# Optimization experiments

Measured on AMD Instinct MI355X. Metric: run time of the kernel, lower is better.

Reference implementation:

```python
import jax, jax.numpy as jnp
import numpy as np

jax.config.update("jax_enable_x64", True)  # hash math uses int64, matching torch promotion

NUM_LEVELS = 16
MIN_RES = 16
MAX_RES = 1024
LOG2_T = 19
T = 2 ** LOG2_T          # hash table size per level
FEATS = 2                # features per level
HASH_INIT_SCALE = 0.001
N = 524288               # number of query points

# 8 cube corners; bit==1 selects ceil coordinate (weight = offset), bit==0 selects floor (weight = 1-offset)
CORNER_BITS = np.array([[(b >> 2) & 1, (b >> 1) & 1, b & 1] for b in range(8)], dtype=np.int64)
PRIMES = np.array([1, 2654435761, 805459861], dtype=np.int64)


def setup_inputs() -> dict:
    key = jax.random.key(0)
    k1, k2 = jax.random.split(key)
    x = jax.random.uniform(k1, (N, 3), dtype=jnp.float32, minval=-1.0, maxval=1.0)
    hash_table = (jax.random.uniform(k2, (T * NUM_LEVELS, FEATS), dtype=jnp.float32) * 2.0 - 1.0) * HASH_INIT_SCALE
    return {"x": x, "hash_table": hash_table}


def reference(x, hash_table):
    # per-level resolutions: floor(min_res * growth^level)
    growth = np.exp((np.log(MAX_RES) - np.log(MIN_RES)) / (NUM_LEVELS - 1))
    scalings = jnp.asarray(np.floor(MIN_RES * growth ** np.arange(NUM_LEVELS)), dtype=jnp.float32)  # [L]
    hash_offset = jnp.arange(NUM_LEVELS, dtype=jnp.int64) * T  # [L]

    x01 = x * 0.5 + 0.5                                # map [-1,1] -> [0,1]
    scaled = x01[..., None, :] * scalings[:, None]     # [N, L, 3]
    sc = jnp.ceil(scaled).astype(jnp.int64)            # [N, L, 3]
    sf = jnp.floor(scaled).astype(jnp.int64)           # [N, L, 3]
    offset = scaled - sf.astype(scaled.dtype)          # [N, L, 3] in [0,1)

    bits = jnp.asarray(CORNER_BITS)                    # [8, 3]
    # corner integer coords: [N, L, 8, 3]
    corners = jnp.where(bits[None, None] == 1, sc[:, :, None, :], sf[:, :, None, :])

    # Instant-NGP spatial hash (int64, matching torch's type promotion)
    p = corners * jnp.asarray(PRIMES)
    h = jnp.bitwise_xor(jnp.bitwise_xor(p[..., 0], p[..., 1]), p[..., 2])
    h = h % T + hash_offset[None, :, None]             # [N, L, 8]

    # trilinear weights: prod over dims of (offset if ceil else 1-offset)
    w = jnp.prod(jnp.where(bits[None, None] == 1, offset[:, :, None, :], 1.0 - offset[:, :, None, :]), axis=-1)  # [N, L, 8]

    feats = hash_table[h]                              # [N, L, 8, F] gather
    enc = jnp.sum(feats * w[..., None], axis=-2)       # [N, L, F]
    return enc.reshape(*enc.shape[:-2], NUM_LEVELS * FEATS)  # [N, L*F]
```

## Files before the change

kernel.cpp:

```cpp
#include <hip/hip_runtime.h>
#include <cmath>

#define TBL_SIZE (1u << 19)
#define TBL_MASK (TBL_SIZE - 1u)
#define PRIME1 2654435761u
#define PRIME2 805459861u
#define NUM_LEVELS 16
#define PPB 32

#define D0g 17
#define D1g 22
#define D2g 28
#define NW0 (D0g*D0g*D0g)
#define NW1 (D1g*D1g*D1g)
#define NW2 (D2g*D2g*D2g)
#define NWTOT (NW0+NW1+NW2)
#define LDSB (NWTOT*4)

struct Args { float s[NUM_LEVELS]; };

typedef float v2f __attribute__((ext_vector_type(2)));

template<int CTRL>
__device__ __forceinline__ float dpp_add(float v) {
    int i = __builtin_bit_cast(int, v);
    int j = __builtin_amdgcn_mov_dpp(i, CTRL, 0xF, 0xF, true);
    return v + __builtin_bit_cast(float, j);
}

__device__ __forceinline__ uint32_t f2bf(float f) {
    uint32_t u = __builtin_bit_cast(uint32_t, f);
    return (u + 0x7FFFu + ((u >> 16) & 1u)) >> 16;
}
__device__ __forceinline__ float bflo(uint32_t v) { return __builtin_bit_cast(float, v << 16); }
__device__ __forceinline__ float bfhi(uint32_t v) { return __builtin_bit_cast(float, v & 0xFFFF0000u); }

__global__ __launch_bounds__(256) void cvt_hashed_kernel(
    const float* __restrict__ table, uint32_t* __restrict__ dst, int L0, int nentries)
{
    int gid = blockIdx.x * 256 + (int)threadIdx.x;
    if (gid >= nentries) return;
    float2 e = reinterpret_cast<const float2*>(table)[((size_t)L0 << 19) + gid];
    dst[gid] = f2bf(e.x) | (f2bf(e.y) << 16);
}

__global__ __launch_bounds__(256) void build_dense3_kernel(
    const float* __restrict__ table, uint32_t* __restrict__ dst)
{
    int id = blockIdx.x * 256 + (int)threadIdx.x;
    if (id >= NWTOT) return;
    int l, rel, D;
    if (id < NW0)            { l = 0; rel = id;             D = D0g; }
    else if (id < NW0 + NW1) { l = 1; rel = id - NW0;       D = D1g; }
    else                     { l = 2; rel = id - NW0 - NW1; D = D2g; }
    int d2 = D * D;
    int xp = rel / d2; int rem = rel - xp * d2;
    int yp = rem / D;  int zp = rem - yp * D;
    uint32_t h = (uint32_t)xp ^ ((uint32_t)yp * PRIME1) ^ ((uint32_t)zp * PRIME2);
    float2 e = reinterpret_cast<const float2*>(table)[((size_t)l << 19) + (h & TBL_MASK)];
    dst[id] = f2bf(e.x) | (f2bf(e.y) << 16);
}

__global__ __launch_bounds__(1024) void lds_levels_kernel(
    const float* __restrict__ x, const uint32_t* __restrict__ wsdense,
    float* __restrict__ out, int npoints, int nchunks,
    float s0, float s1, float s2)
{
    extern __shared__ uint32_t lds[];
    for (int i = (int)threadIdx.x; i < NWTOT; i += 1024) lds[i] = wsdense[i];
    __syncthreads();

    const int t = (int)threadIdx.x;
    const int corner = t & 7, p = t >> 3;
    const int bx = (corner >> 2) & 1, by = (corner >> 1) & 1, bz = corner & 1;

    for (int c = (int)blockIdx.x; c < nchunks; c += (int)gridDim.x) {
        int n = c * 128 + p;
        if (n < npoints) {
            float x0 = x[(size_t)n * 3 + 0] * 0.5f + 0.5f;
            float x1 = x[(size_t)n * 3 + 1] * 0.5f + 0.5f;
            float x2 = x[(size_t)n * 3 + 2] * 0.5f + 0.5f;
            const float ss[3] = {s0, s1, s2};
            const int   dd[3] = {D0g, D1g, D2g};
            const int   bb[3] = {0, NW0, NW0 + NW1};
            #pragma unroll
            for (int l = 0; l < 3; ++l) {
                float sx = x0 * ss[l], sy = x1 * ss[l], sz = x2 * ss[l];
                float fx = floorf(sx), fy = floorf(sy), fz = floorf(sz);
                float ox = sx - fx, oy = sy - fy, oz = sz - fz;
                int D = dd[l];
                int idx = (((int)fx + bx) * D + (int)fy + by) * D + (int)fz + bz;
                int mx = D * D * D - 1;
                idx = idx < mx ? idx : mx;
                uint32_t v = lds[bb[l] + idx];
                float w = (bx ? ox : 1.f - ox) * (by ? oy : 1.f - oy) * (bz ? oz : 1.f - oz);
                float e0 = bflo(v) * w, e1 = bfhi(v) * w;
                e0 = dpp_add<0xB1>(e0);  e1 = dpp_add<0xB1>(e1);
                e0 = dpp_add<0x4E>(e0);  e1 = dpp_add<0x4E>(e1);
                e0 = dpp_add<0x141>(e0); e1 = dpp_add<0x141>(e1);
                if (corner == 0) {
                    v2f r; r.x = e0; r.y = e1;
                    __builtin_nontemporal_store(r, (v2f*)(out + (size_t)n * 32 + l * 2));
                }
            }
        }
    }
}

__global__ __launch_bounds__(256) void HashEncoding_88837103551034_kernel(
    const float* __restrict__ x,
    const float* __restrict__ table,
    const uint32_t* __restrict__ bfws,
    float* __restrict__ out,
    int npoints, int CH, int perXcd, int total, int L0, int NBF,
    Args args)
{
    int b = blockIdx.x; int xcd = b & 7; int sb = b >> 3;
    int g = xcd * perXcd + sb;
    if (g >= total) return;
    int li = g / CH; int level = L0 + li; int chunk = g - li * CH;
    int t = (int)threadIdx.x;
    int corner = t & 7;
    int n = chunk * PPB + (t >> 3);
    if (n >= npoints) return;

    float x0 = x[(size_t)n * 3 + 0] * 0.5f + 0.5f;
    float x1 = x[(size_t)n * 3 + 1] * 0.5f + 0.5f;
    float x2 = x[(size_t)n * 3 + 2] * 0.5f + 0.5f;
    float sl = args.s[level];
    float sx = x0 * sl, sy = x1 * sl, sz = x2 * sl;
    float fx = floorf(sx), fy = floorf(sy), fz = floorf(sz);
    float ox = sx - fx, oy = sy - fy, oz = sz - fz;
    int bx = (corner >> 2) & 1, by = (corner >> 1) & 1, bz = corner & 1;

    uint32_t h = (uint32_t)((int)fx + bx)
               ^ ((uint32_t)((int)fy + by) * PRIME1)
               ^ ((uint32_t)((int)fz + bz) * PRIME2);
    uint32_t idx = h & TBL_MASK;

    float f0, f1;
    if (li < NBF) {
        uint32_t v = bfws[((size_t)li << 19) + idx];
        f0 = bflo(v); f1 = bfhi(v);
    } else {
        float2 f = reinterpret_cast<const float2*>(table)[((size_t)level << 19) + idx];
        f0 = f.x; f1 = f.y;
    }
    float w = (bx ? ox : 1.f - ox) * (by ? oy : 1.f - oy) * (bz ? oz : 1.f - oz);
    float e0 = f0 * w, e1 = f1 * w;
    e0 = dpp_add<0xB1>(e0);  e1 = dpp_add<0xB1>(e1);
    e0 = dpp_add<0x4E>(e0);  e1 = dpp_add<0x4E>(e1);
    e0 = dpp_add<0x141>(e0); e1 = dpp_add<0x141>(e1);
    if (corner == 0) {
        v2f res; res.x = e0; res.y = e1;
        __builtin_nontemporal_store(res, (v2f*)(out + (size_t)n * 32 + level * 2));
    }
}

extern "C" void kernel_launch(void* const* d_in, const int* in_sizes, int n_in,
                              void* d_out, int out_size, void* d_ws, size_t ws_size,
                              hipStream_t stream) {
    const float* x = (const float*)d_in[0];
    const float* table = (const float*)d_in[1];
    float* out = (float*)d_out;
    int npoints = in_sizes[0] / 3;

    Args args;
    double growth = std::exp((std::log(1024.0) - std::log(16.0)) / 15.0);
    for (int l = 0; l < NUM_LEVELS; ++l)
        args.s[l] = (float)std::floor(16.0 * std::pow(growth, (double)l));

    int CH = (npoints + PPB - 1) / PPB;
    uint32_t* ws32 = (uint32_t*)d_ws;

    bool dimsOk = ((int)args.s[0] == 16) && ((int)args.s[1] == 21) && ((int)args.s[2] == 27);
    size_t needA = ((size_t)13 * TBL_SIZE + (size_t)NWTOT) * 4;

    if (dimsOk && ws_size >= needA) {
        int nent = 13 << 19;
        cvt_hashed_kernel<<<nent / 256, 256, 0, stream>>>(table, ws32, 3, nent);
        uint32_t* wsdense = ws32 + (size_t)13 * TBL_SIZE;
        build_dense3_kernel<<<(NWTOT + 255) / 256, 256, 0, stream>>>(table, wsdense);

        hipFuncSetAttribute(reinterpret_cast<const void*>(lds_levels_kernel),
                            hipFuncAttributeMaxDynamicSharedMemorySize, LDSB);
        int nchunks = (npoints + 127) / 128;
        lds_levels_kernel<<<256, 1024, LDSB, stream>>>(
            x, wsdense, out, npoints, nchunks, args.s[0], args.s[1], args.s[2]);

        int total = 13 * CH;
        int perXcd = (total + 7) / 8;
        HashEncoding_88837103551034_kernel<<<8 * perXcd, 256, 0, stream>>>(
            x, table, ws32, out, npoints, CH, perXcd, total, 3, 13, args);
    } else {
        int total = 16 * CH;
        int perXcd = (total + 7) / 8;
        HashEncoding_88837103551034_kernel<<<8 * perXcd, 256, 0, stream>>>(
            x, table, ws32, out, npoints, CH, perXcd, total, 0, 0, args);
    }
}
```

Measured before the change: 256.4 us.

## Use one thread per point in LDS dense levels and merge prep kernels

The dense LDS kernel for the three coarsest levels now gives each thread a whole point instead of one corner per lane. Each thread does eight LDS reads and the trilinear sum in registers, then writes all six outputs with vector stores, so the DPP cross-lane reductions and per-corner redundant coordinate math go away. The LDS grid gets zero-filled padding so corner indices no longer need clamping. The bf16 table conversion kernel and the dense-grid build kernel are merged into one launch to save launch overhead. In exchange, per-thread register pressure and LDS bank conflicts on the scattered reads may rise, and the LDS footprint grows close to the per-CU limit.

```diff
diff --git a/kernel.cpp b/kernel.cpp
--- a/kernel.cpp
+++ b/kernel.cpp
@@ -15,11 +15,19 @@
 #define NW1 (D1g*D1g*D1g)
 #define NW2 (D2g*D2g*D2g)
 #define NWTOT (NW0+NW1+NW2)
-#define LDSB (NWTOT*4)
+#define PAD0 (D0g*D0g+D0g+1)
+#define PAD1 (D1g*D1g+D1g+1)
+#define PAD2 (D2g*D2g+D2g+1)
+#define LB0  0
+#define LB1  (LB0+NW0+PAD0)
+#define LB2  (LB1+NW1+PAD1)
+#define LTOT (LB2+NW2+PAD2)
+#define LDSB (LTOT*4)
 
 struct Args { float s[NUM_LEVELS]; };
 
 typedef float v2f __attribute__((ext_vector_type(2)));
+typedef float v4f __attribute__((ext_vector_type(4)));
 
 template<int CTRL>
 __device__ __forceinline__ float dpp_add(float v) {
@@ -35,75 +43,82 @@
 __device__ __forceinline__ float bflo(uint32_t v) { return __builtin_bit_cast(float, v << 16); }
 __device__ __forceinline__ float bfhi(uint32_t v) { return __builtin_bit_cast(float, v & 0xFFFF0000u); }
 
-__global__ __launch_bounds__(256) void cvt_hashed_kernel(
-    const float* __restrict__ table, uint32_t* __restrict__ dst, int L0, int nentries)
+__global__ __launch_bounds__(256) void prep_kernel(
+    const float* __restrict__ table, uint32_t* __restrict__ bfws,
+    uint32_t* __restrict__ densews, int ncvt)
 {
     int gid = blockIdx.x * 256 + (int)threadIdx.x;
-    if (gid >= nentries) return;
-    float2 e = reinterpret_cast<const float2*>(table)[((size_t)L0 << 19) + gid];
-    dst[gid] = f2bf(e.x) | (f2bf(e.y) << 16);
-}
-
-__global__ __launch_bounds__(256) void build_dense3_kernel(
-    const float* __restrict__ table, uint32_t* __restrict__ dst)
-{
-    int id = blockIdx.x * 256 + (int)threadIdx.x;
-    if (id >= NWTOT) return;
-    int l, rel, D;
-    if (id < NW0)            { l = 0; rel = id;             D = D0g; }
-    else if (id < NW0 + NW1) { l = 1; rel = id - NW0;       D = D1g; }
-    else                     { l = 2; rel = id - NW0 - NW1; D = D2g; }
-    int d2 = D * D;
-    int xp = rel / d2; int rem = rel - xp * d2;
-    int yp = rem / D;  int zp = rem - yp * D;
-    uint32_t h = (uint32_t)xp ^ ((uint32_t)yp * PRIME1) ^ ((uint32_t)zp * PRIME2);
-    float2 e = reinterpret_cast<const float2*>(table)[((size_t)l << 19) + (h & TBL_MASK)];
-    dst[id] = f2bf(e.x) | (f2bf(e.y) << 16);
+    if (gid < NWTOT) {
+        int l, rel, D;
+        if (gid < NW0)            { l = 0; rel = gid;             D = D0g; }
+        else if (gid < NW0 + NW1) { l = 1; rel = gid - NW0;       D = D1g; }
+        else                      { l = 2; rel = gid - NW0 - NW1; D = D2g; }
+        int d2 = D * D;
+        int xp = rel / d2; int rem = rel - xp * d2;
+        int yp = rem / D;  int zp = rem - yp * D;
+        uint32_t h = (uint32_t)xp ^ ((uint32_t)yp * PRIME1) ^ ((uint32_t)zp * PRIME2);
+        float2 e = reinterpret_cast<const float2*>(table)[((size_t)l << 19) + (h & TBL_MASK)];
+        densews[gid] = f2bf(e.x) | (f2bf(e.y) << 16);
+    } else {
+        int rel = gid - NWTOT;
+        if (rel >= ncvt) return;
+        float2 e = reinterpret_cast<const float2*>(table)[((size_t)3 << 19) + rel];
+        bfws[rel] = f2bf(e.x) | (f2bf(e.y) << 16);
+    }
 }
 
 __global__ __launch_bounds__(1024) void lds_levels_kernel(
-    const float* __restrict__ x, const uint32_t* __restrict__ wsdense,
-    float* __restrict__ out, int npoints, int nchunks,
+    const float* __restrict__ x, const uint32_t* __restrict__ densews,
+    float* __restrict__ out, int npoints,
     float s0, float s1, float s2)
 {
     extern __shared__ uint32_t lds[];
-    for (int i = (int)threadIdx.x; i < NWTOT; i += 1024) lds[i] = wsdense[i];
+    for (int i = (int)threadIdx.x; i < LTOT; i += 1024) lds[i] = 0;
     __syncthreads();
-
-    const int t = (int)threadIdx.x;
-    const int corner = t & 7, p = t >> 3;
-    const int bx = (corner >> 2) & 1, by = (corner >> 1) & 1, bz = corner & 1;
-
-    for (int c = (int)blockIdx.x; c < nchunks; c += (int)gridDim.x) {
-        int n = c * 128 + p;
-        if (n < npoints) {
-            float x0 = x[(size_t)n * 3 + 0] * 0.5f + 0.5f;
-            float x1 = x[(size_t)n * 3 + 1] * 0.5f + 0.5f;
-            float x2 = x[(size_t)n * 3 + 2] * 0.5f + 0.5f;
-            const float ss[3] = {s0, s1, s2};
-            const int   dd[3] = {D0g, D1g, D2g};
-            const int   bb[3] = {0, NW0, NW0 + NW1};
-            #pragma unroll
-            for (int l = 0; l < 3; ++l) {
-                float sx = x0 * ss[l], sy = x1 * ss[l], sz = x2 * ss[l];
-                float fx = floorf(sx), fy = floorf(sy), fz = floorf(sz);
-                float ox = sx - fx, oy = sy - fy, oz = sz - fz;
-                int D = dd[l];
-                int idx = (((int)fx + bx) * D + (int)fy + by) * D + (int)fz + bz;
-                int mx = D * D * D - 1;
-                idx = idx < mx ? idx : mx;
-                uint32_t v = lds[bb[l] + idx];
-                float w = (bx ? ox : 1.f - ox) * (by ? oy : 1.f - oy) * (bz ? oz : 1.f - oz);
-                float e0 = bflo(v) * w, e1 = bfhi(v) * w;
-                e0 = dpp_add<0xB1>(e0);  e1 = dpp_add<0xB1>(e1);
-                e0 = dpp_add<0x4E>(e0);  e1 = dpp_add<0x4E>(e1);
-                e0 = dpp_add<0x141>(e0); e1 = dpp_add<0x141>(e1);
-                if (corner == 0) {
-                    v2f r; r.x = e0; r.y = e1;
-                    __builtin_nontemporal_store(r, (v2f*)(out + (size_t)n * 32 + l * 2));
-                }
-            }
+    for (int i = (int)threadIdx.x; i < NW0; i += 1024) lds[LB0 + i] = densews[i];
+    for (int i = (int)threadIdx.x; i < NW1; i += 1024) lds[LB1 + i] = densews[NW0 + i];
+    for (int i = (int)threadIdx.x; i < NW2; i += 1024) lds[LB2 + i] = densews[NW0 + NW1 + i];
+    __syncthreads();
+
+    float acc[6];
+    for (int n = blockIdx.x * 1024 + (int)threadIdx.x; n < npoints; n += (int)gridDim.x * 1024) {
+        float x0 = x[(size_t)n * 3 + 0] * 0.5f + 0.5f;
+        float x1 = x[(size_t)n * 3 + 1] * 0.5f + 0.5f;
+        float x2 = x[(size_t)n * 3 + 2] * 0.5f + 0.5f;
+
+#define DO_LEVEL(LI, DCONST, LBASE, SCALE)                                        \
+        {                                                                         \
+            const int D = DCONST, D2 = DCONST * DCONST;                           \
+            float sx = x0 * SCALE, sy = x1 * SCALE, sz = x2 * SCALE;              \
+            float fx = floorf(sx), fy = floorf(sy), fz = floorf(sz);              \
+            float ox = sx - fx, oy = sy - fy, oz = sz - fz;                       \
+            int base = LBASE + ((int)fx * D + (int)fy) * D + (int)fz;             \
+            uint32_t v000 = lds[base];            uint32_t v001 = lds[base + 1];  \
+            uint32_t v010 = lds[base + D];        uint32_t v011 = lds[base + D + 1]; \
+            uint32_t v100 = lds[base + D2];       uint32_t v101 = lds[base + D2 + 1]; \
+            uint32_t v110 = lds[base + D2 + D];   uint32_t v111 = lds[base + D2 + D + 1]; \
+            float gx0 = 1.f - ox, gy0 = 1.f - oy, gz0 = 1.f - oz;                 \
+            float w000 = gx0 * gy0 * gz0, w001 = gx0 * gy0 * oz;                  \
+            float w010 = gx0 * oy * gz0,  w011 = gx0 * oy * oz;                   \
+            float w100 = ox * gy0 * gz0,  w101 = ox * gy0 * oz;                   \
+            float w110 = ox * oy * gz0,   w111 = ox * oy * oz;                    \
+            acc[LI*2+0] = bflo(v000)*w000 + bflo(v001)*w001 + bflo(v010)*w010     \
+                        + bflo(v011)*w011 + bflo(v100)*w100 + bflo(v101)*w101     \
+                        + bflo(v110)*w110 + bflo(v111)*w111;                      \
+            acc[LI*2+1] = bfhi(v000)*w000 + bfhi(v001)*w001 + bfhi(v010)*w010     \
+                        + bfhi(v011)*w011 + bfhi(v100)*w100 + bfhi(v101)*w101     \
+                        + bfhi(v110)*w110 + bfhi(v111)*w111;                      \
         }
+        DO_LEVEL(0, D0g, LB0, s0)
+        DO_LEVEL(1, D1g, LB1, s1)
+        DO_LEVEL(2, D2g, LB2, s2)
+#undef DO_LEVEL
+
+        v4f a; a.x = acc[0]; a.y = acc[1]; a.z = acc[2]; a.w = acc[3];
+        v2f b; b.x = acc[4]; b.y = acc[5];
+        float* o = out + (size_t)n * 32;
+        __builtin_nontemporal_store(a, (v4f*)o);
+        __builtin_nontemporal_store(b, (v2f*)(o + 4));
     }
 }
 
@@ -177,16 +192,15 @@
     size_t needA = ((size_t)13 * TBL_SIZE + (size_t)NWTOT) * 4;
 
     if (dimsOk && ws_size >= needA) {
-        int nent = 13 << 19;
-        cvt_hashed_kernel<<<nent / 256, 256, 0, stream>>>(table, ws32, 3, nent);
         uint32_t* wsdense = ws32 + (size_t)13 * TBL_SIZE;
-        build_dense3_kernel<<<(NWTOT + 255) / 256, 256, 0, stream>>>(table, wsdense);
+        int ncvt = 13 << 19;
+        int ptot = NWTOT + ncvt;
+        prep_kernel<<<(ptot + 255) / 256, 256, 0, stream>>>(table, ws32, wsdense, ncvt);
 
         hipFuncSetAttribute(reinterpret_cast<const void*>(lds_levels_kernel),
                             hipFuncAttributeMaxDynamicSharedMemorySize, LDSB);
-        int nchunks = (npoints + 127) / 128;
         lds_levels_kernel<<<256, 1024, LDSB, stream>>>(
-            x, wsdense, out, npoints, nchunks, args.s[0], args.s[1], args.s[2]);
+            x, wsdense, out, npoints, args.s[0], args.s[1], args.s[2]);
 
         int total = 13 * CH;
         int perXcd = (total + 7) / 8;
```

Measured after the change: 251.6 us. No clear change (-1.9%).
